# Kernel optimization log

Hardware: AMD Instinct MI355X
Metric: run time of the kernel (lower is better)

The kernel has to match this reference:

```python
import jax, jax.numpy as jnp
import numpy as np

GAMMA = 0.99
GAE_LAMBDA = 0.95
CLIP = 0.2
ENT_COEF = 0.01
VF_COEF = 0.5


def setup_inputs() -> dict:
    key = jax.random.key(0)
    ks = jax.random.split(key, 12)
    T, D, H, A = 65536, 512, 256, 16
    obs = jax.random.normal(ks[0], (T, D), dtype=jnp.float32)
    actions = jax.random.randint(ks[1], (T,), 0, A, dtype=jnp.int32)
    logprobs = jax.random.normal(ks[2], (T,), dtype=jnp.float32)
    rewards = jax.random.normal(ks[3], (T,), dtype=jnp.float32)
    terms = jax.random.uniform(ks[4], (T,), dtype=jnp.float32)
    values = jax.random.normal(ks[5], (T,), dtype=jnp.float32)
    # orthogonal-init-like scaling (std sqrt(2) for trunk, 0.01 actor, 1.0 critic)
    W1 = jax.random.normal(ks[6], (D, H), dtype=jnp.float32) * np.float32(np.sqrt(2.0 / D))
    b1 = jnp.zeros((H,), jnp.float32)
    W2 = jax.random.normal(ks[7], (H, H), dtype=jnp.float32) * np.float32(np.sqrt(2.0 / H))
    b2 = jnp.zeros((H,), jnp.float32)
    Wa = jax.random.normal(ks[8], (H, A), dtype=jnp.float32) * np.float32(0.01 / np.sqrt(H))
    ba = jnp.zeros((A,), jnp.float32)
    Wc = jax.random.normal(ks[9], (H, 1), dtype=jnp.float32) * np.float32(1.0 / np.sqrt(H))
    bc = jnp.zeros((1,), jnp.float32)
    return {"obs": obs, "actions": actions, "logprobs": logprobs, "rewards": rewards,
            "terms": terms, "values": values, "W1": W1, "b1": b1, "W2": W2, "b2": b2,
            "Wa": Wa, "ba": ba, "Wc": Wc, "bc": bc}


def reference(obs, actions, logprobs, rewards, terms, values,
              W1, b1, W2, b2, Wa, ba, Wc, bc):
    # ---- GAE (torch.no_grad in original -> stop_gradient) ----
    nonterm = 1.0 - terms                                   # [T]
    next_vals = jnp.concatenate([values[1:], jnp.zeros((1,), values.dtype)])
    delta = rewards + GAMMA * next_vals * nonterm - values  # [T]

    def step(carry, x):  # reverse recurrence a_t = d_t + g*l*nt_t * a_{t+1}
        d, nt = x
        g = d + GAMMA * GAE_LAMBDA * nt * carry
        return g, g

    _, adv = jax.lax.scan(step, jnp.float32(0.0), (delta, nonterm), reverse=True)
    adv = jax.lax.stop_gradient(adv)
    returns = adv + jax.lax.stop_gradient(values)
    vals_old = jax.lax.stop_gradient(values)

    # ---- actor-critic MLP (get_action_and_value) ----
    hidden = jnp.tanh(jnp.tanh(obs @ W1 + b1) @ W2 + b2)    # [T,256]
    logits = hidden @ Wa + ba                               # [T,A]
    logp = jax.nn.log_softmax(logits, axis=-1)
    newlp = jnp.take_along_axis(logp, actions[:, None].astype(jnp.int32), axis=1)[:, 0]
    entropy = -jnp.sum(jnp.exp(logp) * logp, axis=-1)       # [T]
    value = (hidden @ Wc + bc)[:, 0]                        # [T]

    # ---- clipped PPO losses (single full-batch minibatch) ----
    ratio = jnp.exp(newlp - logprobs)
    a = (adv - adv.mean()) / (adv.std() + 1e-8)
    pg_loss = jnp.maximum(-a * ratio, -a * jnp.clip(ratio, 1.0 - CLIP, 1.0 + CLIP)).mean()
    v_clipped = vals_old + jnp.clip(value - vals_old, -CLIP, CLIP)
    v_loss = 0.5 * jnp.maximum((value - returns) ** 2, (v_clipped - returns) ** 2).mean()
    loss = pg_loss - ENT_COEF * entropy.mean() + VF_COEF * v_loss
    return loss
```

## Files before the change

### kernel.cpp

```cpp
#include <hip/hip_runtime.h>


#define TT 65536

typedef float f32x4 __attribute__((ext_vector_type(4)));
typedef __bf16 bf16x8 __attribute__((ext_vector_type(8)));
typedef unsigned short u16x8 __attribute__((ext_vector_type(8)));
typedef unsigned short u16x4 __attribute__((ext_vector_type(4)));

__device__ __forceinline__ unsigned short f2bf(float f) {
    unsigned int u = __float_as_uint(f);
    unsigned int r = (u + 0x7fffu + ((u >> 16) & 1u)) >> 16;
    return (unsigned short)r;
}

__device__ __forceinline__ float fast_tanh(float x) {
    float e = __expf(2.0f * x);
    return fmaf(-2.0f, __builtin_amdgcn_rcpf(e + 1.0f), 1.0f);
}

__device__ __forceinline__ void async_lds16(void* lds, const void* g) {
    __builtin_amdgcn_global_load_lds(
        (const __attribute__((address_space(1))) unsigned int*)g,
        (__attribute__((address_space(3))) unsigned int*)lds, 16, 0, 0);
}

__device__ __forceinline__ void suffix_scan256(float* sC, float* sD, int i) {
    float c = sC[i], d = sD[i];
#pragma unroll
    for (int s = 1; s < 256; s <<= 1) {
        float c2 = 1.0f, d2 = 0.0f;
        if (i + s < 256) { c2 = sC[i + s]; d2 = sD[i + s]; }
        __syncthreads();
        d = d + c * d2;
        c = c * c2;
        sC[i] = c; sD[i] = d;
        __syncthreads();
    }
}

__device__ __forceinline__ void gae_cd(const float* rewards, const float* terms,
                                       const float* values, int t, float* c, float* d) {
    float nt = 1.0f - terms[t];
    float nv = (t + 1 < TT) ? values[t + 1] : 0.0f;
    *d = rewards[t] + 0.99f * nv * nt - values[t];
    *c = 0.99f * 0.95f * nt;
}

__global__ void k_prep_gae1(const float* __restrict__ W1, const float* __restrict__ W2,
                            const float* __restrict__ Wa, const float* __restrict__ Wc,
                            unsigned short* __restrict__ W1T, unsigned short* __restrict__ W2T,
                            unsigned short* __restrict__ WavT,
                            const float* __restrict__ rewards, const float* __restrict__ terms,
                            const float* __restrict__ values, float* __restrict__ aggC,
                            float* __restrict__ aggD) {
    if (blockIdx.x < 800) {
        int idx = blockIdx.x * 256 + threadIdx.x;
        if (idx < 131072) {
            int kt = idx >> 13;
            int L = (idx & 8191) >> 3, e = idx & 7;
            int row = L >> 2, p = L & 3;
            int k = kt * 32 + (((p ^ ((row >> 1) & 3)) << 3) | e);
            W1T[idx] = f2bf(W1[k * 256 + row]);
        } else if (idx < 196608) {
            int i = idx - 131072;
            int kt = i >> 13;
            int L = (i & 8191) >> 3, e = i & 7;
            int row = L >> 2, p = L & 3;
            int k = kt * 32 + (((p ^ ((row >> 1) & 3)) << 3) | e);
            W2T[i] = f2bf(W2[k * 256 + row]);
        } else if (idx < 204800) {
            int i = idx - 196608;
            int L = i >> 3, e = i & 7;
            int row = L >> 5, ec = (L & 31) << 3;
            int k = ((ec ^ ((row & 7) << 3)) | e);
            float v = (row < 16) ? Wa[k * 16 + row] : ((row == 16) ? Wc[k] : 0.0f);
            WavT[i] = f2bf(v);
        }
        return;
    }
    __shared__ float sC[256], sD[256];
    int i = threadIdx.x;
    int b = blockIdx.x - 800;
    int t = b * 256 + i;
    float c, d;
    gae_cd(rewards, terms, values, t, &c, &d);
    sC[i] = c; sD[i] = d;
    __syncthreads();
    suffix_scan256(sC, sD, i);
    if (i == 0) { aggC[b] = sC[0]; aggD[b] = sD[0]; }
}

__global__ void k_gae3(const float* __restrict__ rewards, const float* __restrict__ terms,
                       const float* __restrict__ values, const float* __restrict__ aggC,
                       const float* __restrict__ aggD, float* __restrict__ adv,
                       float* __restrict__ ret, float* __restrict__ sumP) {
    __shared__ float sC[256], sD[256];
    int i = threadIdx.x, b = blockIdx.x;
    sC[i] = aggC[i]; sD[i] = aggD[i];
    __syncthreads();
    suffix_scan256(sC, sD, i);
    float carry = (b < 255) ? sD[b + 1] : 0.0f;
    __syncthreads();

    int t = b * 256 + i;
    float c, d;
    gae_cd(rewards, terms, values, t, &c, &d);
    sC[i] = c; sD[i] = d;
    __syncthreads();
    suffix_scan256(sC, sD, i);
    float a = sD[i] + sC[i] * carry;
    adv[t] = a;
    ret[t] = a + values[t];
    __syncthreads();
    sC[i] = a; sD[i] = a * a;
    __syncthreads();
#pragma unroll
    for (int s = 128; s > 0; s >>= 1) {
        if (i < s) { sC[i] += sC[i + s]; sD[i] += sD[i + s]; }
        __syncthreads();
    }
    if (i == 0) { sumP[2 * b] = sC[0]; sumP[2 * b + 1] = sD[0]; }
}

__global__ __launch_bounds__(512, 4) void k_mlp(
    const float* __restrict__ obs, const int* __restrict__ actions,
    const float* __restrict__ logprobs, const float* __restrict__ values,
    const float* __restrict__ b1, const float* __restrict__ b2,
    const float* __restrict__ ba, const float* __restrict__ bc,
    const unsigned short* __restrict__ W1T, const unsigned short* __restrict__ W2T,
    const unsigned short* __restrict__ WavT, const float* __restrict__ adv,
    const float* __restrict__ ret, const float* __restrict__ sumP,
    float* __restrict__ lossP) {
    __shared__ __align__(16) unsigned char SM[73728];
    unsigned short* smB = (unsigned short*)SM;
    unsigned short* smA = (unsigned short*)(SM + 32768);
    unsigned short* smH = (unsigned short*)(SM + 40960);
    float* red = (float*)(SM + 40960);
    float* red2 = (float*)(SM + 32768);

    const int tid = threadIdx.x;
    const int wid = tid >> 6;
    const int lane = tid & 63;
    const int cl = lane & 15;
    const int gg = lane >> 4;
    const int bm0 = blockIdx.x * 64;

    const int arow = tid >> 3;
    const int acol = (tid & 7) * 4;
    const int adst = arow * 32 +
        ((((acol >> 3) ^ ((arow >> 1) & 3)) << 3) | (acol & 4));
    const float* aSrc = obs + (size_t)(bm0 + arow) * 512 + acol;

    float4 areg = *(const float4*)aSrc;
#pragma unroll
    for (int c = 0; c < 2; ++c) {
        int chunk = wid * 2 + c;
        async_lds16(&smB[chunk * 512], W1T + chunk * 512 + lane * 8);
    }

    float meanA, rstdA;
    {
        if (tid < 256) { red[tid] = sumP[2 * tid]; red[256 + tid] = sumP[2 * tid + 1]; }
        __syncthreads();
#pragma unroll
        for (int s = 128; s > 0; s >>= 1) {
            if (tid < s) { red[tid] += red[tid + s]; red[256 + tid] += red[256 + tid + s]; }
            __syncthreads();
        }
        meanA = red[0] * (1.0f / TT);
        float var = red[256] * (1.0f / TT) - meanA * meanA;
        rstdA = 1.0f / (sqrtf(fmaxf(var, 0.0f)) + 1e-8f);
        __syncthreads();
    }

    float b1v[2], b2v[2];
#pragma unroll
    for (int n = 0; n < 2; ++n) {
        int c = wid * 32 + n * 16 + cl;
        b1v[n] = b1[c];
        b2v[n] = b2[c];
    }
    const float bav = ba[cl];
    const float bc0 = bc[0];

    f32x4 acc[4][2];
#pragma unroll
    for (int m = 0; m < 4; ++m)
#pragma unroll
        for (int n = 0; n < 2; ++n) acc[m][n] = (f32x4){0.f, 0.f, 0.f, 0.f};

    auto writeA = [&](int buf) {
        u16x4 ac;
        ac[0] = f2bf(areg.x); ac[1] = f2bf(areg.y);
        ac[2] = f2bf(areg.z); ac[3] = f2bf(areg.w);
        *(u16x4*)&smA[buf * 2048 + adst] = ac;
    };

    writeA(0);
    __syncthreads();

#pragma unroll
    for (int t = 0; t < 16; ++t) {
        const unsigned short* bsrc = (t < 15) ? (W1T + (t + 1) * 8192) : W2T;
#pragma unroll
        for (int c = 0; c < 2; ++c) {
            int chunk = wid * 2 + c;
            async_lds16(&smB[((t + 1) & 1) * 8192 + chunk * 512], bsrc + chunk * 512 + lane * 8);
        }
        if (t < 15) areg = *(const float4*)(aSrc + (t + 1) * 32);

        bf16x8 av[4], bv[2];
#pragma unroll
        for (int m = 0; m < 4; ++m) {
            int ra = m * 16 + cl;
            av[m] = *(const bf16x8*)&smA[(t & 1) * 2048 + ra * 32 + ((gg ^ ((ra >> 1) & 3)) << 3)];
        }
#pragma unroll
        for (int n = 0; n < 2; ++n) {
            int rb = wid * 32 + n * 16 + cl;
            bv[n] = *(const bf16x8*)&smB[(t & 1) * 8192 + rb * 32 + ((gg ^ ((rb >> 1) & 3)) << 3)];
        }
#pragma unroll
        for (int m = 0; m < 4; ++m)
#pragma unroll
            for (int n = 0; n < 2; ++n)
                acc[m][n] = __builtin_amdgcn_mfma_f32_16x16x32_bf16(av[m], bv[n], acc[m][n], 0, 0, 0);
        if (t < 15) writeA((t + 1) & 1);
        __syncthreads();
    }

#pragma unroll
    for (int m = 0; m < 4; ++m)
#pragma unroll
        for (int n = 0; n < 2; ++n)
#pragma unroll
            for (int j = 0; j < 4; ++j) {
                int r = m * 16 + gg * 4 + j;
                int c = wid * 32 + n * 16 + cl;
                smH[r * 256 + (c ^ ((r & 7) << 3))] = f2bf(fast_tanh(acc[m][n][j] + b1v[n]));
                acc[m][n][j] = 0.0f;
            }
    __syncthreads();

#pragma unroll
    for (int t = 0; t < 8; ++t) {
        const unsigned short* bsrc = (t < 7) ? (W2T + (t + 1) * 8192) : WavT;
#pragma unroll
        for (int c = 0; c < 2; ++c) {
            int chunk = wid * 2 + c;
            async_lds16(&smB[((t + 1) & 1) * 8192 + chunk * 512], bsrc + chunk * 512 + lane * 8);
        }
        bf16x8 av[4], bv[2];
#pragma unroll
        for (int m = 0; m < 4; ++m) {
            int ra = m * 16 + cl;
            av[m] = *(const bf16x8*)&smH[ra * 256 + ((t * 32 + gg * 8) ^ ((ra & 7) << 3))];
        }
#pragma unroll
        for (int n = 0; n < 2; ++n) {
            int rb = wid * 32 + n * 16 + cl;
            bv[n] = *(const bf16x8*)&smB[(t & 1) * 8192 + rb * 32 + ((gg ^ ((rb >> 1) & 3)) << 3)];
        }
#pragma unroll
        for (int m = 0; m < 4; ++m)
#pragma unroll
            for (int n = 0; n < 2; ++n)
                acc[m][n] = __builtin_amdgcn_mfma_f32_16x16x32_bf16(av[m], bv[n], acc[m][n], 0, 0, 0);
        __syncthreads();
    }

#pragma unroll
    for (int m = 0; m < 4; ++m)
#pragma unroll
        for (int n = 0; n < 2; ++n)
#pragma unroll
            for (int j = 0; j < 4; ++j) {
                int r = m * 16 + gg * 4 + j;
                int c = wid * 32 + n * 16 + cl;
                smH[r * 256 + (c ^ ((r & 7) << 3))] = f2bf(fast_tanh(acc[m][n][j] + b2v[n]));
            }
    __syncthreads();

    float lsum = 0.0f;
    if (wid < 4) {
        f32x4 acc_a = {0.f, 0.f, 0.f, 0.f}, acc_v = {0.f, 0.f, 0.f, 0.f};
#pragma unroll
        for (int kk = 0; kk < 8; ++kk) {
            int r = wid * 16 + cl;
            bf16x8 av = *(const bf16x8*)&smH[r * 256 + ((kk * 32 + gg * 8) ^ ((r & 7) << 3))];
            int ra2 = cl;
            bf16x8 bva = *(const bf16x8*)&smB[ra2 * 256 + ((kk * 32 + gg * 8) ^ ((ra2 & 7) << 3))];
            int rv = 16 + cl;
            bf16x8 bvv = *(const bf16x8*)&smB[rv * 256 + ((kk * 32 + gg * 8) ^ ((rv & 7) << 3))];
            acc_a = __builtin_amdgcn_mfma_f32_16x16x32_bf16(av, bva, acc_a, 0, 0, 0);
            acc_v = __builtin_amdgcn_mfma_f32_16x16x32_bf16(av, bvv, acc_v, 0, 0, 0);
        }

        const int t0 = bm0 + wid * 16;
#pragma unroll
        for (int j = 0; j < 4; ++j) {
            int t = t0 + gg * 4 + j;
            float lg = acc_a[j] + bav;
            float mx = lg;
#pragma unroll
            for (int dd = 1; dd < 16; dd <<= 1) mx = fmaxf(mx, __shfl_xor(mx, dd));
            float ex = __expf(lg - mx);
            float se = ex;
#pragma unroll
            for (int dd = 1; dd < 16; dd <<= 1) se += __shfl_xor(se, dd);
            float ls = __logf(se);
            float lp = lg - mx - ls;
            float pl = __expf(lp) * lp;
            float ent = pl;
#pragma unroll
            for (int dd = 1; dd < 16; dd <<= 1) ent += __shfl_xor(ent, dd);
            ent = -ent;
            int act = actions[t];
            float newlp = __shfl(lp, (lane & 48) | act);
            float val = __shfl(acc_v[j], lane & 48) + bc0;

            float lpo = logprobs[t];
            float at = (adv[t] - meanA) * rstdA;
            float rt = ret[t];
            float vo = values[t];
            float ratio = __expf(newlp - lpo);
            float rcl = fminf(fmaxf(ratio, 0.8f), 1.2f);
            float pg = fmaxf(-at * ratio, -at * rcl);
            float vcl = vo + fminf(fmaxf(val - vo, -0.2f), 0.2f);
            float dv = val - rt, dvc = vcl - rt;
            float vl = fmaxf(dv * dv, dvc * dvc);
            if (cl == 0) lsum += pg - 0.01f * ent + 0.25f * vl;
        }
        lsum += __shfl_xor(lsum, 16);
        lsum += __shfl_xor(lsum, 32);
    }
    __syncthreads();
    if (wid < 4 && lane == 0) red2[wid] = lsum;
    __syncthreads();
    if (tid == 0) lossP[blockIdx.x] = red2[0] + red2[1] + red2[2] + red2[3];
}

__global__ void k_final(const float* __restrict__ lossP, float* __restrict__ out) {
    __shared__ float s[256];
    int i = threadIdx.x;
    s[i] = lossP[i] + lossP[i + 256] + lossP[i + 512] + lossP[i + 768];
    __syncthreads();
#pragma unroll
    for (int st = 128; st > 0; st >>= 1) {
        if (i < st) s[i] += s[i + st];
        __syncthreads();
    }
    if (i == 0) out[0] = s[0] * (1.0f / TT);
}

extern "C" void kernel_launch(void* const* d_in, const int* in_sizes, int n_in,
                              void* d_out, int out_size, void* d_ws, size_t ws_size,
                              hipStream_t stream) {
    const float* obs      = (const float*)d_in[0];
    const int*   actions  = (const int*)d_in[1];
    const float* logprobs = (const float*)d_in[2];
    const float* rewards  = (const float*)d_in[3];
    const float* terms    = (const float*)d_in[4];
    const float* values   = (const float*)d_in[5];
    const float* W1 = (const float*)d_in[6];
    const float* b1 = (const float*)d_in[7];
    const float* W2 = (const float*)d_in[8];
    const float* b2 = (const float*)d_in[9];
    const float* Wa = (const float*)d_in[10];
    const float* ba = (const float*)d_in[11];
    const float* Wc = (const float*)d_in[12];
    const float* bc = (const float*)d_in[13];

    char* ws = (char*)d_ws;
    unsigned short* W1T  = (unsigned short*)(ws + 0);
    unsigned short* W2T  = (unsigned short*)(ws + 262144);
    unsigned short* WavT = (unsigned short*)(ws + 393216);
    float* advp  = (float*)(ws + 409600);
    float* retp  = (float*)(ws + 671744);
    float* aggC  = (float*)(ws + 933888);
    float* aggD  = (float*)(ws + 934912);
    float* sumP  = (float*)(ws + 936960);
    float* lossP = (float*)(ws + 939072);

    k_prep_gae1<<<1056, 256, 0, stream>>>(W1, W2, Wa, Wc, W1T, W2T, WavT,
                                          rewards, terms, values, aggC, aggD);
    k_gae3<<<256, 256, 0, stream>>>(rewards, terms, values, aggC, aggD, advp, retp, sumP);
    k_mlp<<<1024, 512, 0, stream>>>(obs, actions, logprobs, values, b1, b2, ba, bc,
                                    W1T, W2T, WavT, advp, retp, sumP, lossP);
    k_final<<<1, 256, 0, stream>>>(lossP, (float*)d_out);
}
```

Measured before the change: 65.90 us.

## Use 256-thread MLP blocks without double buffering to cut LDS and raise occupancy

The MLP kernel moves from 512 to 256 threads per block. Each wave now covers 64 output columns instead of 32, with a 4x4 MFMA accumulator tile. The double-buffered weight and activation staging in LDS becomes a single buffer with a sync before compute, shrinking shared memory from 72KB to 52KB so more blocks can be resident. The cost is that loads no longer overlap with MFMA inside a block, so latency hiding now depends on other resident blocks, and the larger accumulator tile raises register pressure.

```diff
diff --git a/kernel.cpp b/kernel.cpp
--- a/kernel.cpp
+++ b/kernel.cpp
@@ -123,7 +123,7 @@
     if (i == 0) { sumP[2 * b] = sC[0]; sumP[2 * b + 1] = sD[0]; }
 }
 
-__global__ __launch_bounds__(512, 4) void k_mlp(
+__global__ __launch_bounds__(256, 3) void k_mlp(
     const float* __restrict__ obs, const int* __restrict__ actions,
     const float* __restrict__ logprobs, const float* __restrict__ values,
     const float* __restrict__ b1, const float* __restrict__ b2,
@@ -132,12 +132,12 @@
     const unsigned short* __restrict__ WavT, const float* __restrict__ adv,
     const float* __restrict__ ret, const float* __restrict__ sumP,
     float* __restrict__ lossP) {
-    __shared__ __align__(16) unsigned char SM[73728];
+    __shared__ __align__(16) unsigned char SM[53248];
     unsigned short* smB = (unsigned short*)SM;
-    unsigned short* smA = (unsigned short*)(SM + 32768);
-    unsigned short* smH = (unsigned short*)(SM + 40960);
-    float* red = (float*)(SM + 40960);
-    float* red2 = (float*)(SM + 32768);
+    unsigned short* smA = (unsigned short*)(SM + 16384);
+    unsigned short* smH = (unsigned short*)(SM + 20480);
+    float* red = (float*)(SM + 20480);
+    float* red2 = (float*)(SM + 16384);
 
     const int tid = threadIdx.x;
     const int wid = tid >> 6;
@@ -146,22 +146,15 @@
     const int gg = lane >> 4;
     const int bm0 = blockIdx.x * 64;
 
-    const int arow = tid >> 3;
-    const int acol = (tid & 7) * 4;
-    const int adst = arow * 32 +
-        ((((acol >> 3) ^ ((arow >> 1) & 3)) << 3) | (acol & 4));
-    const float* aSrc = obs + (size_t)(bm0 + arow) * 512 + acol;
-
-    float4 areg = *(const float4*)aSrc;
-#pragma unroll
-    for (int c = 0; c < 2; ++c) {
-        int chunk = wid * 2 + c;
-        async_lds16(&smB[chunk * 512], W1T + chunk * 512 + lane * 8);
-    }
+    const int arow = tid >> 2;
+    const int aslot = tid & 3;
+    const int adst = arow * 32 + ((aslot ^ ((arow >> 1) & 3)) << 3);
+    const float* aSrc = obs + (size_t)(bm0 + arow) * 512 + aslot * 8;
 
     float meanA, rstdA;
     {
-        if (tid < 256) { red[tid] = sumP[2 * tid]; red[256 + tid] = sumP[2 * tid + 1]; }
+        red[tid] = sumP[2 * tid];
+        red[256 + tid] = sumP[2 * tid + 1];
         __syncthreads();
 #pragma unroll
         for (int s = 128; s > 0; s >>= 1) {
@@ -174,116 +167,121 @@
         __syncthreads();
     }
 
-    float b1v[2], b2v[2];
-#pragma unroll
-    for (int n = 0; n < 2; ++n) {
-        int c = wid * 32 + n * 16 + cl;
+    float b1v[4], b2v[4];
+#pragma unroll
+    for (int n = 0; n < 4; ++n) {
+        int c = wid * 64 + n * 16 + cl;
         b1v[n] = b1[c];
         b2v[n] = b2[c];
     }
     const float bav = ba[cl];
     const float bc0 = bc[0];
 
-    f32x4 acc[4][2];
+    f32x4 acc[4][4];
 #pragma unroll
     for (int m = 0; m < 4; ++m)
 #pragma unroll
-        for (int n = 0; n < 2; ++n) acc[m][n] = (f32x4){0.f, 0.f, 0.f, 0.f};
-
-    auto writeA = [&](int buf) {
-        u16x4 ac;
-        ac[0] = f2bf(areg.x); ac[1] = f2bf(areg.y);
-        ac[2] = f2bf(areg.z); ac[3] = f2bf(areg.w);
-        *(u16x4*)&smA[buf * 2048 + adst] = ac;
-    };
-
-    writeA(0);
-    __syncthreads();
-
-#pragma unroll
+        for (int n = 0; n < 4; ++n) acc[m][n] = (f32x4){0.f, 0.f, 0.f, 0.f};
+
     for (int t = 0; t < 16; ++t) {
-        const unsigned short* bsrc = (t < 15) ? (W1T + (t + 1) * 8192) : W2T;
-#pragma unroll
-        for (int c = 0; c < 2; ++c) {
-            int chunk = wid * 2 + c;
-            async_lds16(&smB[((t + 1) & 1) * 8192 + chunk * 512], bsrc + chunk * 512 + lane * 8);
-        }
-        if (t < 15) areg = *(const float4*)(aSrc + (t + 1) * 32);
-
-        bf16x8 av[4], bv[2];
+        {
+            const unsigned short* bsrc = W1T + t * 8192 + lane * 8;
+#pragma unroll
+            for (int c = 0; c < 4; ++c) {
+                int chunk = wid * 4 + c;
+                async_lds16(&smB[chunk * 512], bsrc + chunk * 512);
+            }
+            float4 a0 = *(const float4*)(aSrc + t * 32);
+            float4 a1 = *(const float4*)(aSrc + t * 32 + 4);
+            u16x8 cc;
+            cc[0] = f2bf(a0.x); cc[1] = f2bf(a0.y); cc[2] = f2bf(a0.z); cc[3] = f2bf(a0.w);
+            cc[4] = f2bf(a1.x); cc[5] = f2bf(a1.y); cc[6] = f2bf(a1.z); cc[7] = f2bf(a1.w);
+            *(u16x8*)&smA[adst] = cc;
+        }
+        __syncthreads();
+        bf16x8 av[4], bv[4];
 #pragma unroll
         for (int m = 0; m < 4; ++m) {
             int ra = m * 16 + cl;
-            av[m] = *(const bf16x8*)&smA[(t & 1) * 2048 + ra * 32 + ((gg ^ ((ra >> 1) & 3)) << 3)];
-        }
-#pragma unroll
-        for (int n = 0; n < 2; ++n) {
-            int rb = wid * 32 + n * 16 + cl;
-            bv[n] = *(const bf16x8*)&smB[(t & 1) * 8192 + rb * 32 + ((gg ^ ((rb >> 1) & 3)) << 3)];
+            av[m] = *(const bf16x8*)&smA[ra * 32 + ((gg ^ ((ra >> 1) & 3)) << 3)];
+        }
+#pragma unroll
+        for (int n = 0; n < 4; ++n) {
+            int rb = wid * 64 + n * 16 + cl;
+            bv[n] = *(const bf16x8*)&smB[rb * 32 + ((gg ^ ((rb >> 1) & 3)) << 3)];
         }
 #pragma unroll
         for (int m = 0; m < 4; ++m)
 #pragma unroll
-            for (int n = 0; n < 2; ++n)
+            for (int n = 0; n < 4; ++n)
                 acc[m][n] = __builtin_amdgcn_mfma_f32_16x16x32_bf16(av[m], bv[n], acc[m][n], 0, 0, 0);
-        if (t < 15) writeA((t + 1) & 1);
         __syncthreads();
     }
 
 #pragma unroll
     for (int m = 0; m < 4; ++m)
 #pragma unroll
-        for (int n = 0; n < 2; ++n)
+        for (int n = 0; n < 4; ++n)
 #pragma unroll
             for (int j = 0; j < 4; ++j) {
                 int r = m * 16 + gg * 4 + j;
-                int c = wid * 32 + n * 16 + cl;
+                int c = wid * 64 + n * 16 + cl;
                 smH[r * 256 + (c ^ ((r & 7) << 3))] = f2bf(fast_tanh(acc[m][n][j] + b1v[n]));
                 acc[m][n][j] = 0.0f;
             }
     __syncthreads();
 
-#pragma unroll
     for (int t = 0; t < 8; ++t) {
-        const unsigned short* bsrc = (t < 7) ? (W2T + (t + 1) * 8192) : WavT;
-#pragma unroll
-        for (int c = 0; c < 2; ++c) {
-            int chunk = wid * 2 + c;
-            async_lds16(&smB[((t + 1) & 1) * 8192 + chunk * 512], bsrc + chunk * 512 + lane * 8);
-        }
-        bf16x8 av[4], bv[2];
+        {
+            const unsigned short* bsrc = W2T + t * 8192 + lane * 8;
+#pragma unroll
+            for (int c = 0; c < 4; ++c) {
+                int chunk = wid * 4 + c;
+                async_lds16(&smB[chunk * 512], bsrc + chunk * 512);
+            }
+        }
+        __syncthreads();
+        bf16x8 av[4], bv[4];
 #pragma unroll
         for (int m = 0; m < 4; ++m) {
             int ra = m * 16 + cl;
             av[m] = *(const bf16x8*)&smH[ra * 256 + ((t * 32 + gg * 8) ^ ((ra & 7) << 3))];
         }
 #pragma unroll
-        for (int n = 0; n < 2; ++n) {
-            int rb = wid * 32 + n * 16 + cl;
-            bv[n] = *(const bf16x8*)&smB[(t & 1) * 8192 + rb * 32 + ((gg ^ ((rb >> 1) & 3)) << 3)];
+        for (int n = 0; n < 4; ++n) {
+            int rb = wid * 64 + n * 16 + cl;
+            bv[n] = *(const bf16x8*)&smB[rb * 32 + ((gg ^ ((rb >> 1) & 3)) << 3)];
         }
 #pragma unroll
         for (int m = 0; m < 4; ++m)
 #pragma unroll
-            for (int n = 0; n < 2; ++n)
+            for (int n = 0; n < 4; ++n)
                 acc[m][n] = __builtin_amdgcn_mfma_f32_16x16x32_bf16(av[m], bv[n], acc[m][n], 0, 0, 0);
         __syncthreads();
     }
 
+    {
+        const unsigned short* bsrc = WavT + lane * 8;
+#pragma unroll
+        for (int c = 0; c < 4; ++c) {
+            int chunk = wid * 4 + c;
+            async_lds16(&smB[chunk * 512], bsrc + chunk * 512);
+        }
+    }
 #pragma unroll
     for (int m = 0; m < 4; ++m)
 #pragma unroll
-        for (int n = 0; n < 2; ++n)
+        for (int n = 0; n < 4; ++n)
 #pragma unroll
             for (int j = 0; j < 4; ++j) {
                 int r = m * 16 + gg * 4 + j;
-                int c = wid * 32 + n * 16 + cl;
+                int c = wid * 64 + n * 16 + cl;
                 smH[r * 256 + (c ^ ((r & 7) << 3))] = f2bf(fast_tanh(acc[m][n][j] + b2v[n]));
             }
     __syncthreads();
 
     float lsum = 0.0f;
-    if (wid < 4) {
+    {
         f32x4 acc_a = {0.f, 0.f, 0.f, 0.f}, acc_v = {0.f, 0.f, 0.f, 0.f};
 #pragma unroll
         for (int kk = 0; kk < 8; ++kk) {
@@ -336,7 +334,7 @@
         lsum += __shfl_xor(lsum, 32);
     }
     __syncthreads();
-    if (wid < 4 && lane == 0) red2[wid] = lsum;
+    if (lane == 0) red2[wid] = lsum;
     __syncthreads();
     if (tid == 0) lossP[blockIdx.x] = red2[0] + red2[1] + red2[2] + red2[3];
 }
@@ -386,7 +384,7 @@
     k_prep_gae1<<<1056, 256, 0, stream>>>(W1, W2, Wa, Wc, W1T, W2T, WavT,
                                           rewards, terms, values, aggC, aggD);
     k_gae3<<<256, 256, 0, stream>>>(rewards, terms, values, aggC, aggD, advp, retp, sumP);
-    k_mlp<<<1024, 512, 0, stream>>>(obs, actions, logprobs, values, b1, b2, ba, bc,
+    k_mlp<<<1024, 256, 0, stream>>>(obs, actions, logprobs, values, b1, b2, ba, bc,
                                     W1T, W2T, WavT, advp, retp, sumP, lossP);
     k_final<<<1, 256, 0, stream>>>(lossP, (float*)d_out);
 }
```

Measured after the change: 80.01 us. 1.21x slower.
